# Kernel tuning notes

Hardware: AMD Instinct MI355X
Metric: run time of the kernel (lower is better)

Reference implementation:

```python
import jax, jax.numpy as jnp
import numpy as np

N, E, H = 100000, 640000, 64
DIN_N, DIN_E, L, OUT = 32, 16, 2, 1
BN_EPS = 1e-5


def setup_inputs() -> dict:
    key = jax.random.key(0)
    ks = iter(jax.random.split(key, 40))
    def p(shape, s=0.05):
        return jax.random.normal(next(ks), shape, dtype=jnp.float32) * s
    return {
        "x": jax.random.normal(next(ks), (N, DIN_N), dtype=jnp.float32),
        "edge_attr": jax.random.normal(next(ks), (E, DIN_E), dtype=jnp.float32),
        "src": jax.random.randint(next(ks), (E,), 0, N),
        "dst": jax.random.randint(next(ks), (E,), 0, N),
        "node_emb_w": p((DIN_N, H)), "node_emb_b": p((H,)),
        "edge_emb_w": p((DIN_E, H)), "edge_emb_b": p((H,)),
        "lin_edge_w": p((L, H, H)), "lin_edge_b": p((L, H)),
        "conv_w1": p((L, H, H)), "conv_b1": p((L, H)),
        "conv_w2": p((L, H, H)), "conv_b2": p((L, H)),
        "emlp_w1": p((L, 3 * H, H)), "emlp_b1": p((L, H)),
        "emlp_w2": p((L, H, H)), "emlp_b2": p((L, H)),
        "bn_gamma": jnp.ones((L, H), jnp.float32),
        "bn_beta": jnp.zeros((L, H), jnp.float32),
        "mlp_w1": p((3 * H, 50)), "mlp_b1": p((50,)),
        "mlp_w2": p((50, 25)), "mlp_b2": p((25,)),
        "mlp_w3": p((25, OUT)), "mlp_b3": p((OUT,)),
    }


def _batchnorm(h, gamma, beta):
    # training-mode BatchNorm1d over the node axis (biased variance)
    mu = jnp.mean(h, axis=0)
    var = jnp.mean(jnp.square(h - mu), axis=0)
    return gamma * (h - mu) * jax.lax.rsqrt(var + BN_EPS) + beta


def _forward(x, edge_attr, src, dst,
             node_emb_w, node_emb_b, edge_emb_w, edge_emb_b,
             lin_edge_w, lin_edge_b, conv_w1, conv_b1, conv_w2, conv_b2,
             emlp_w1, emlp_b1, emlp_w2, emlp_b2, bn_gamma, bn_beta,
             mlp_w1, mlp_b1, mlp_w2, mlp_b2, mlp_w3, mlp_b3):
    x = x @ node_emb_w + node_emb_b                       # [N, H]
    e = edge_attr @ edge_emb_w + edge_emb_b               # [E, H]
    for i in range(L):
        # GINEConv (eps=0): msg = ReLU(x_src + Lin(edge_attr)); sum at dst
        msg = jax.nn.relu(x[src] + e @ lin_edge_w[i] + lin_edge_b[i])
        agg = jax.ops.segment_sum(msg, dst, num_segments=N)
        h = x + agg
        h = jax.nn.relu(h @ conv_w1[i] + conv_b1[i]) @ conv_w2[i] + conv_b2[i]
        x = (x + jax.nn.relu(_batchnorm(h, bn_gamma[i], bn_beta[i]))) / 2
        cat = jnp.concatenate([x[src], x[dst], e], axis=-1)  # [E, 3H]
        upd = jax.nn.relu(cat @ emlp_w1[i] + emlp_b1[i]) @ emlp_w2[i] + emlp_b2[i]
        e = e + upd / 2
    # edge readout: relu(cat(x_src, x_dst)) ++ edge_attr -> MLP (dropout off/eval)
    er = jnp.concatenate(
        [jax.nn.relu(jnp.concatenate([x[src], x[dst]], axis=-1)), e], axis=-1)
    hmid = jax.nn.relu(er @ mlp_w1 + mlp_b1)
    hmid = jax.nn.relu(hmid @ mlp_w2 + mlp_b2)
    logit = hmid @ mlp_w3 + mlp_b3
    return x, logit


def reference(x, edge_attr, src, dst,
              node_emb_w, node_emb_b, edge_emb_w, edge_emb_b,
              lin_edge_w, lin_edge_b, conv_w1, conv_b1, conv_w2, conv_b2,
              emlp_w1, emlp_b1, emlp_w2, emlp_b2, bn_gamma, bn_beta,
              mlp_w1, mlp_b1, mlp_w2, mlp_b2, mlp_w3, mlp_b3):
    return _forward(x, edge_attr, src, dst,
                    node_emb_w, node_emb_b, edge_emb_w, edge_emb_b,
                    lin_edge_w, lin_edge_b, conv_w1, conv_b1, conv_w2, conv_b2,
                    emlp_w1, emlp_b1, emlp_w2, emlp_b2, bn_gamma, bn_beta,
                    mlp_w1, mlp_b1, mlp_w2, mlp_b2, mlp_w3, mlp_b3)
```

## Files before the change

### kernel.cpp

```cpp
#include <hip/hip_runtime.h>

#define NN 100000
#define NE 640000
#define NB_SCAN 98

typedef __attribute__((ext_vector_type(8))) short short8;
typedef __attribute__((ext_vector_type(4))) float f32x4;
typedef __attribute__((ext_vector_type(4))) ushort ushort4v;

__device__ __forceinline__ float bf2f(ushort u) {
    unsigned v = ((unsigned)u) << 16;
    return __builtin_bit_cast(float, v);
}
__device__ __forceinline__ ushort f2bf(float f) {
    unsigned u = __builtin_bit_cast(unsigned, f);
    u += 0x7fffu + ((u >> 16) & 1u);
    return (ushort)(u >> 16);
}
__device__ __forceinline__ short8 brelu(short8 v) {
    #pragma unroll
    for (int i = 0; i < 8; ++i) v[i] = (v[i] < (short)0) ? (short)0 : v[i];
    return v;
}

__global__ void k_hist(const int* __restrict__ dst, int* __restrict__ hist)
{
    int i = blockIdx.x * 256 + threadIdx.x;
    atomicAdd(&hist[dst[i]], 1);
}

__global__ __launch_bounds__(256) void k_scan_part(const int* __restrict__ hist,
                                                   int* __restrict__ rp,
                                                   int* __restrict__ parts)
{
    __shared__ int s[256];
    int b = blockIdx.x, t = threadIdx.x;
    int base = b * 1024 + t * 4;
    int v[4]; int sum = 0;
    #pragma unroll
    for (int i = 0; i < 4; ++i) { int idx = base + i; v[i] = (idx < NN) ? hist[idx] : 0; sum += v[i]; }
    s[t] = sum; __syncthreads();
    for (int off = 1; off < 256; off <<= 1) {
        int x = (t >= off) ? s[t - off] : 0;
        __syncthreads(); s[t] += x; __syncthreads();
    }
    int excl = s[t] - sum;
    if (t == 255) parts[b] = s[255];
    int run = excl;
    #pragma unroll
    for (int i = 0; i < 4; ++i) { int idx = base + i; if (idx < NN) rp[idx] = run; run += v[i]; }
}

__global__ void k_scan_tops(int* __restrict__ parts, int* __restrict__ rp)
{
    __shared__ int s[128];
    int t = threadIdx.x;
    int v = (t < NB_SCAN) ? parts[t] : 0;
    s[t] = v; __syncthreads();
    for (int off = 1; off < 128; off <<= 1) {
        int x = (t >= off) ? s[t - off] : 0;
        __syncthreads(); s[t] += x; __syncthreads();
    }
    parts[t] = s[t] - v;
    if (t == 0) rp[NN] = NE;
}

__global__ __launch_bounds__(256) void k_scan_add(int* __restrict__ rp,
                                                  const int* __restrict__ parts,
                                                  int* __restrict__ cursor)
{
    int i = blockIdx.x * 256 + threadIdx.x;
    if (i >= NN) return;
    int v = rp[i] + parts[i >> 10];
    rp[i] = v; cursor[i] = v;
}

__global__ void k_scatter(const int* __restrict__ dst,
                          int* __restrict__ cursor, int* __restrict__ eidx)
{
    int i = blockIdx.x * 256 + threadIdx.x;
    int d = dst[i];
    int p = atomicAdd(&cursor[d], 1);
    eidx[p] = i;
}

__global__ void k_w_subtile(const float* __restrict__ w, ushort* __restrict__ out,
                            int K, int Nin)
{
    int t = blockIdx.x * 256 + threadIdx.x;
    if (t >= K * 64) return;
    int k = t >> 6, c = t & 63;
    float v = (c < Nin) ? w[k * Nin + c] : 0.f;
    out[((k >> 3) * 64 + c) * 8 + (k & 7)] = f2bf(v);
}

__global__ void k_w_padk(const float* __restrict__ w, ushort* __restrict__ out,
                         int Kreal, int Kpad)
{
    int t = blockIdx.x * 256 + threadIdx.x;
    if (t >= Kpad * 64) return;
    int k = t >> 6, c = t & 63;
    float v = (k < Kreal) ? w[k * 64 + c] : 0.f;
    out[((k >> 3) * 64 + c) * 8 + (k & 7)] = f2bf(v);
}

__global__ void k_w_msg(const float* __restrict__ lw, ushort* __restrict__ out)
{
    int t = blockIdx.x * 256 + threadIdx.x;
    if (t >= 128 * 64) return;
    int k = t >> 6, c = t & 63;
    float v = (k < 64) ? (k == c ? 1.f : 0.f) : lw[(k - 64) * 64 + c];
    out[((k >> 3) * 64 + c) * 8 + (k & 7)] = f2bf(v);
}

__global__ __launch_bounds__(256) void k_node_emb_mfma(
    const float* __restrict__ xin, const ushort* __restrict__ ws,
    const float* __restrict__ b, float* __restrict__ xout,
    ushort* __restrict__ xb)
{
    __shared__ ushort wl[32 * 64];
    __shared__ float fbuf[4][16 * 64];
    __shared__ ushort bbuf[4][16 * 64];
    int tid = threadIdx.x;
    *(short8*)&wl[tid * 8] = *(const short8*)&ws[tid * 8];
    __syncthreads();

    int wid = tid >> 6, lane = tid & 63, c = lane & 15, kg = lane >> 4;
    int t = blockIdx.x * 4 + wid;
    if (t >= NN / 16) return;
    int n0 = t * 16;

    const float* xr = xin + (size_t)(n0 + c) * 32 + kg * 8;
    f32x4 u0 = *(const f32x4*)xr, u1 = *(const f32x4*)(xr + 4);
    short8 a;
    #pragma unroll
    for (int j = 0; j < 4; ++j) { a[j] = (short)f2bf(u0[j]); a[4 + j] = (short)f2bf(u1[j]); }

    f32x4 acc[4];
    #pragma unroll
    for (int nt = 0; nt < 4; ++nt) {
        float bv = b[nt * 16 + c];
        acc[nt] = f32x4{bv, bv, bv, bv};
        short8 bf = *(const short8*)&wl[(kg * 64 + nt * 16 + c) * 8];
        acc[nt] = __builtin_amdgcn_mfma_f32_16x16x32_bf16(a, bf, acc[nt], 0, 0, 0);
    }
    #pragma unroll
    for (int nt = 0; nt < 4; ++nt)
        #pragma unroll
        for (int i = 0; i < 4; ++i) {
            int rr = kg * 4 + i, cc = nt * 16 + c;
            float v = acc[nt][i];
            fbuf[wid][rr * 64 + cc] = v;
            bbuf[wid][rr * 64 + cc] = f2bf(v);
        }
    #pragma unroll
    for (int r = 0; r < 4; ++r) {
        int q = r * 64 + lane;
        *(f32x4*)&xout[(size_t)(n0 + (q >> 4)) * 64 + (q & 15) * 4] =
            *(f32x4*)&fbuf[wid][q * 4];
    }
    #pragma unroll
    for (int r = 0; r < 2; ++r) {
        int q = r * 64 + lane;
        *(short8*)&xb[(size_t)(n0 + (q >> 3)) * 64 + (q & 7) * 8] =
            *(short8*)&bbuf[wid][q * 8];
    }
}

__global__ __launch_bounds__(256) void k_edge_emb_fused(
    const float* __restrict__ ein, const ushort* __restrict__ ws,
    const float* __restrict__ b, ushort* __restrict__ eb,
    const ushort* __restrict__ xb, const int* __restrict__ src,
    const ushort* __restrict__ wm, const float* __restrict__ lb,
    ushort* __restrict__ msgbuf)
{
    __shared__ ushort wl[32 * 64];
    __shared__ ushort wml[128 * 64];
    __shared__ ushort bbuf[4][16 * 72];
    int tid = threadIdx.x;
    *(short8*)&wl[tid * 8] = *(const short8*)&ws[tid * 8];
    #pragma unroll
    for (int i = 0; i < 4; ++i)
        *(short8*)&wml[(i * 256 + tid) * 8] = *(const short8*)&wm[(i * 256 + tid) * 8];
    __syncthreads();

    int wid = tid >> 6, lane = tid & 63, c = lane & 15, kg = lane >> 4;
    int e0 = (blockIdx.x * 4 + wid) * 16;
    ushort* bb = bbuf[wid];

    short8 a = (short8)0;
    if (kg < 2) {
        const float* er = ein + (size_t)(e0 + c) * 16 + kg * 8;
        f32x4 u0 = *(const f32x4*)er, u1 = *(const f32x4*)(er + 4);
        #pragma unroll
        for (int j = 0; j < 4; ++j) { a[j] = (short)f2bf(u0[j]); a[4 + j] = (short)f2bf(u1[j]); }
    }
    f32x4 acc[4];
    #pragma unroll
    for (int nt = 0; nt < 4; ++nt) {
        float bv = b[nt * 16 + c];
        acc[nt] = f32x4{bv, bv, bv, bv};
        short8 bf = *(const short8*)&wl[(kg * 64 + nt * 16 + c) * 8];
        acc[nt] = __builtin_amdgcn_mfma_f32_16x16x32_bf16(a, bf, acc[nt], 0, 0, 0);
    }
    #pragma unroll
    for (int nt = 0; nt < 4; ++nt)
        #pragma unroll
        for (int i = 0; i < 4; ++i)
            bb[(kg * 4 + i) * 72 + nt * 16 + c] = f2bf(acc[nt][i]);
    #pragma unroll
    for (int r = 0; r < 2; ++r) {
        int q = r * 64 + lane;
        *(short8*)&eb[(size_t)(e0 + (q >> 3)) * 64 + (q & 7) * 8] =
            *(short8*)&bb[(q >> 3) * 72 + (q & 7) * 8];
    }
    short8 en0 = *(const short8*)&bb[c * 72 + kg * 8];
    short8 en1 = *(const short8*)&bb[c * 72 + 32 + kg * 8];
    const ushort* xs = xb + (size_t)src[e0 + c] * 64;
    short8 a0 = *(const short8*)(xs + kg * 8);
    short8 a1 = *(const short8*)(xs + 32 + kg * 8);

    f32x4 acc3[4];
    #pragma unroll
    for (int nt = 0; nt < 4; ++nt) {
        float bv = lb[nt * 16 + c];
        acc3[nt] = f32x4{bv, bv, bv, bv};
    }
    short8 af[4] = {a0, a1, en0, en1};
    #pragma unroll
    for (int ks = 0; ks < 4; ++ks) {
        #pragma unroll
        for (int nt = 0; nt < 4; ++nt) {
            short8 bf = *(const short8*)&wml[((ks * 4 + kg) * 64 + nt * 16 + c) * 8];
            acc3[nt] = __builtin_amdgcn_mfma_f32_16x16x32_bf16(af[ks], bf, acc3[nt], 0, 0, 0);
        }
    }
    #pragma unroll
    for (int nt = 0; nt < 4; ++nt)
        #pragma unroll
        for (int i = 0; i < 4; ++i)
            bb[(kg * 4 + i) * 72 + nt * 16 + c] = f2bf(fmaxf(acc3[nt][i], 0.f));
    #pragma unroll
    for (int r = 0; r < 2; ++r) {
        int q = r * 64 + lane;
        *(short8*)&msgbuf[(size_t)(e0 + (q >> 3)) * 64 + (q & 7) * 8] =
            *(short8*)&bb[(q >> 3) * 72 + (q & 7) * 8];
    }
}

__global__ __launch_bounds__(256) void k_conv_csr(
    const float* __restrict__ x, const ushort* __restrict__ msgbuf,
    const int* __restrict__ rp, const int* __restrict__ eidx,
    float* __restrict__ hout,
    const ushort* __restrict__ w1s, const float* __restrict__ b1,
    const ushort* __restrict__ w2s, const float* __restrict__ b2,
    float* __restrict__ stats)
{
    __shared__ ushort w1l[64 * 64];
    __shared__ ushort w2l[64 * 64];
    __shared__ ushort h1l[4][1024];
    __shared__ float red[2][4][64];
    int tid = threadIdx.x;
    #pragma unroll
    for (int i = 0; i < 2; ++i) {
        *(short8*)&w1l[(i * 256 + tid) * 8] = *(const short8*)&w1s[(i * 256 + tid) * 8];
        *(short8*)&w2l[(i * 256 + tid) * 8] = *(const short8*)&w2s[(i * 256 + tid) * 8];
    }
    __syncthreads();

    int wid = tid >> 6, lane = tid & 63;
    int c = lane & 15, kg = lane >> 4;

    short8 w2f[2][4];
    #pragma unroll
    for (int ks = 0; ks < 2; ++ks)
        #pragma unroll
        for (int nt = 0; nt < 4; ++nt)
            w2f[ks][nt] = *(const short8*)&w2l[((ks * 4 + kg) * 64 + nt * 16 + c) * 8];

    float b1v[4], b2v[4];
    #pragma unroll
    for (int nt = 0; nt < 4; ++nt) { b1v[nt] = b1[nt * 16 + c]; b2v[nt] = b2[nt * 16 + c]; }

    float s1[4] = {0.f, 0.f, 0.f, 0.f}, s2[4] = {0.f, 0.f, 0.f, 0.f};
    ushort* hl = h1l[wid];

    int t = blockIdx.x * 4 + wid;
    if (t < NN / 16) {
        int n0 = t * 16;
        int n = n0 + c;
        int jb = rp[n], je = rp[n + 1];
        float sm0[8] = {0,0,0,0,0,0,0,0}, sm1[8] = {0,0,0,0,0,0,0,0};
        for (int j = jb; j < je; ++j) {
            int row = eidx[j];
            short8 m0 = *(const short8*)&msgbuf[(size_t)row * 64 + kg * 8];
            short8 m1 = *(const short8*)&msgbuf[(size_t)row * 64 + 32 + kg * 8];
            #pragma unroll
            for (int i = 0; i < 8; ++i) {
                sm0[i] += bf2f((ushort)m0[i]);
                sm1[i] += bf2f((ushort)m1[i]);
            }
        }
        const float* xr = x + (size_t)n * 64;
        f32x4 u0 = *(const f32x4*)(xr + kg * 8);
        f32x4 u1 = *(const f32x4*)(xr + kg * 8 + 4);
        f32x4 v0 = *(const f32x4*)(xr + 32 + kg * 8);
        f32x4 v1 = *(const f32x4*)(xr + 32 + kg * 8 + 4);
        short8 a[2];
        #pragma unroll
        for (int j = 0; j < 4; ++j) {
            a[0][j]     = (short)f2bf(u0[j] + sm0[j]);
            a[0][4 + j] = (short)f2bf(u1[j] + sm0[4 + j]);
            a[1][j]     = (short)f2bf(v0[j] + sm1[j]);
            a[1][4 + j] = (short)f2bf(v1[j] + sm1[4 + j]);
        }
        f32x4 acc[4];
        #pragma unroll
        for (int nt = 0; nt < 4; ++nt) acc[nt] = f32x4{b1v[nt], b1v[nt], b1v[nt], b1v[nt]};
        #pragma unroll
        for (int ks = 0; ks < 2; ++ks) {
            #pragma unroll
            for (int nt = 0; nt < 4; ++nt) {
                short8 bf = *(const short8*)&w1l[((ks * 4 + kg) * 64 + nt * 16 + c) * 8];
                acc[nt] = __builtin_amdgcn_mfma_f32_16x16x32_bf16(a[ks], bf, acc[nt], 0, 0, 0);
            }
        }
        #pragma unroll
        for (int nt = 0; nt < 4; ++nt) {
            #pragma unroll
            for (int i = 0; i < 4; ++i) {
                int rr = kg * 4 + i, cc = nt * 16 + c;
                hl[((cc >> 3) * 16 + rr) * 8 + (cc & 7)] = f2bf(fmaxf(acc[nt][i], 0.f));
            }
        }
        f32x4 acc2[4];
        #pragma unroll
        for (int nt = 0; nt < 4; ++nt) acc2[nt] = f32x4{b2v[nt], b2v[nt], b2v[nt], b2v[nt]};
        #pragma unroll
        for (int ks = 0; ks < 2; ++ks) {
            short8 ha = *(const short8*)&hl[((ks * 4 + kg) * 16 + c) * 8];
            #pragma unroll
            for (int nt = 0; nt < 4; ++nt)
                acc2[nt] = __builtin_amdgcn_mfma_f32_16x16x32_bf16(ha, w2f[ks][nt], acc2[nt], 0, 0, 0);
        }
        #pragma unroll
        for (int nt = 0; nt < 4; ++nt) {
            #pragma unroll
            for (int i = 0; i < 4; ++i) {
                int rr = kg * 4 + i, cc = nt * 16 + c;
                float h2 = acc2[nt][i];
                hout[(size_t)(n0 + rr) * 64 + cc] = h2;
                s1[nt] += h2;
                s2[nt] += h2 * h2;
            }
        }
    }
    #pragma unroll
    for (int nt = 0; nt < 4; ++nt) {
        float v1 = s1[nt], v2 = s2[nt];
        v1 += __shfl_xor(v1, 16); v1 += __shfl_xor(v1, 32);
        v2 += __shfl_xor(v2, 16); v2 += __shfl_xor(v2, 32);
        s1[nt] = v1; s2[nt] = v2;
    }
    if (lane < 16) {
        #pragma unroll
        for (int nt = 0; nt < 4; ++nt) {
            red[0][wid][nt * 16 + c] = s1[nt];
            red[1][wid][nt * 16 + c] = s2[nt];
        }
    }
    __syncthreads();
    if (wid == 0) {
        float a = red[0][0][lane] + red[0][1][lane] + red[0][2][lane] + red[0][3][lane];
        float b = red[1][0][lane] + red[1][1][lane] + red[1][2][lane] + red[1][3][lane];
        unsafeAtomicAdd(&stats[lane], a);
        unsafeAtomicAdd(&stats[64 + lane], b);
    }
}

__global__ void k_bnfin(float* __restrict__ stats,
                        const float* __restrict__ gamma,
                        const float* __restrict__ beta)
{
    int j = threadIdx.x;
    float mu = stats[j] * (1.f / NN);
    float var = stats[64 + j] * (1.f / NN) - mu * mu;
    float a = gamma[j] * rsqrtf(var + 1e-5f);
    stats[128 + j] = a;
    stats[192 + j] = beta[j] - mu * a;
}

__global__ __launch_bounds__(256) void k_xupd4(float* __restrict__ x,
                                               const float* __restrict__ h,
                                               const float* __restrict__ stats,
                                               ushort* __restrict__ xb)
{
    int idx = blockIdx.x * 256 + threadIdx.x;
    int j4 = (idx & 15) * 4;
    f32x4 hv = *(const f32x4*)&h[(size_t)idx * 4];
    f32x4 xv = *(const f32x4*)&x[(size_t)idx * 4];
    f32x4 av = *(const f32x4*)&stats[128 + j4];
    f32x4 cv = *(const f32x4*)&stats[192 + j4];
    f32x4 xo;
    ushort4v bo;
    #pragma unroll
    for (int i = 0; i < 4; ++i) {
        float r = fmaxf(fmaf(hv[i], av[i], cv[i]), 0.f);
        float xn = (xv[i] + r) * 0.5f;
        xo[i] = xn;
        bo[i] = f2bf(xn);
    }
    *(f32x4*)&x[(size_t)idx * 4] = xo;
    *(ushort4v*)&xb[(size_t)idx * 4] = bo;
}

template<int NEXT>
__global__ __launch_bounds__(256) void k_emlp_fused(
    const ushort* __restrict__ xb, ushort* __restrict__ eb,
    const int* __restrict__ src, const int* __restrict__ dst,
    const ushort* __restrict__ w1s, const float* __restrict__ b1,
    const ushort* __restrict__ w2s, const float* __restrict__ b2,
    const ushort* __restrict__ wm, const float* __restrict__ lbn,
    ushort* __restrict__ msgbuf)
{
    __shared__ ushort w1l[192 * 64];
    __shared__ ushort wml[NEXT ? 128 * 64 : 8];
    __shared__ ushort hb[4][1152];
    int tid = threadIdx.x;
    #pragma unroll
    for (int i = 0; i < 6; ++i)
        *(short8*)&w1l[(i * 256 + tid) * 8] = *(const short8*)&w1s[(i * 256 + tid) * 8];
    if (NEXT) {
        #pragma unroll
        for (int i = 0; i < 4; ++i)
            *(short8*)&wml[(i * 256 + tid) * 8] = *(const short8*)&wm[(i * 256 + tid) * 8];
    }
    __syncthreads();

    int wid = tid >> 6, lane = tid & 63;
    int c = lane & 15, kg = lane >> 4;

    short8 w2f[2][4];
    #pragma unroll
    for (int ks = 0; ks < 2; ++ks)
        #pragma unroll
        for (int nt = 0; nt < 4; ++nt)
            w2f[ks][nt] = *(const short8*)&w2s[((ks * 4 + kg) * 64 + nt * 16 + c) * 8];

    float b1v[4], b2v[4], lbv[4];
    #pragma unroll
    for (int nt = 0; nt < 4; ++nt) {
        b1v[nt] = b1[nt * 16 + c];
        b2v[nt] = b2[nt * 16 + c];
        lbv[nt] = NEXT ? lbn[nt * 16 + c] : 0.f;
    }
    ushort* hl = hb[wid];

    #pragma unroll 1
    for (int t4 = 0; t4 < 4; ++t4) {
        int e0 = blockIdx.x * 256 + wid * 64 + t4 * 16;
        int myedge = e0 + c;
        int s = src[myedge], d = dst[myedge];
        const ushort* xs = xb + (size_t)s * 64;
        const ushort* xd = xb + (size_t)d * 64;
        const ushort* ee = eb + (size_t)myedge * 64;
        short8 a[6];
        a[0] = *(const short8*)(xs + kg * 8);
        a[1] = *(const short8*)(xs + 32 + kg * 8);
        a[2] = *(const short8*)(xd + kg * 8);
        a[3] = *(const short8*)(xd + 32 + kg * 8);
        a[4] = *(const short8*)(ee + kg * 8);
        a[5] = *(const short8*)(ee + 32 + kg * 8);

        f32x4 acc[4];
        #pragma unroll
        for (int nt = 0; nt < 4; ++nt) acc[nt] = f32x4{b1v[nt], b1v[nt], b1v[nt], b1v[nt]};
        #pragma unroll
        for (int ks = 0; ks < 6; ++ks) {
            #pragma unroll
            for (int nt = 0; nt < 4; ++nt) {
                short8 bf = *(const short8*)&w1l[((ks * 4 + kg) * 64 + nt * 16 + c) * 8];
                acc[nt] = __builtin_amdgcn_mfma_f32_16x16x32_bf16(a[ks], bf, acc[nt], 0, 0, 0);
            }
        }
        #pragma unroll
        for (int nt = 0; nt < 4; ++nt) {
            #pragma unroll
            for (int i = 0; i < 4; ++i) {
                int rr = kg * 4 + i, cc = nt * 16 + c;
                hl[((cc >> 3) * 16 + rr) * 8 + (cc & 7)] = f2bf(fmaxf(acc[nt][i], 0.f));
            }
        }
        f32x4 acc2[4];
        #pragma unroll
        for (int nt = 0; nt < 4; ++nt) acc2[nt] = f32x4{b2v[nt], b2v[nt], b2v[nt], b2v[nt]};
        #pragma unroll
        for (int ks = 0; ks < 2; ++ks) {
            short8 ha = *(const short8*)&hl[((ks * 4 + kg) * 16 + c) * 8];
            #pragma unroll
            for (int nt = 0; nt < 4; ++nt)
                acc2[nt] = __builtin_amdgcn_mfma_f32_16x16x32_bf16(ha, w2f[ks][nt], acc2[nt], 0, 0, 0);
        }
        #pragma unroll
        for (int nt = 0; nt < 4; ++nt)
            #pragma unroll
            for (int i = 0; i < 4; ++i)
                hl[(kg * 4 + i) * 72 + nt * 16 + c] = f2bf(acc2[nt][i]);
        short8 u0 = *(const short8*)&hl[c * 72 + kg * 8];
        short8 u1 = *(const short8*)&hl[c * 72 + 32 + kg * 8];
        short8 en0, en1;
        #pragma unroll
        for (int j = 0; j < 8; ++j) {
            en0[j] = (short)f2bf(bf2f((ushort)a[4][j]) + 0.5f * bf2f((ushort)u0[j]));
            en1[j] = (short)f2bf(bf2f((ushort)a[5][j]) + 0.5f * bf2f((ushort)u1[j]));
        }
        *(short8*)&eb[(size_t)myedge * 64 + kg * 8]      = en0;
        *(short8*)&eb[(size_t)myedge * 64 + 32 + kg * 8] = en1;

        if (NEXT) {
            f32x4 acc3[4];
            #pragma unroll
            for (int nt = 0; nt < 4; ++nt) acc3[nt] = f32x4{lbv[nt], lbv[nt], lbv[nt], lbv[nt]};
            short8 af[4] = {a[0], a[1], en0, en1};
            #pragma unroll
            for (int ks = 0; ks < 4; ++ks) {
                #pragma unroll
                for (int nt = 0; nt < 4; ++nt) {
                    short8 bf = *(const short8*)&wml[((ks * 4 + kg) * 64 + nt * 16 + c) * 8];
                    acc3[nt] = __builtin_amdgcn_mfma_f32_16x16x32_bf16(af[ks], bf, acc3[nt], 0, 0, 0);
                }
            }
            #pragma unroll
            for (int nt = 0; nt < 4; ++nt)
                #pragma unroll
                for (int i = 0; i < 4; ++i)
                    hl[(kg * 4 + i) * 72 + nt * 16 + c] = f2bf(fmaxf(acc3[nt][i], 0.f));
            #pragma unroll
            for (int r = 0; r < 2; ++r) {
                int q = r * 64 + lane;
                *(short8*)&msgbuf[(size_t)(e0 + (q >> 3)) * 64 + (q & 7) * 8] =
                    *(short8*)&hl[(q >> 3) * 72 + (q & 7) * 8];
            }
        }
    }
}

__global__ __launch_bounds__(256) void k_readout_mfma(
    const ushort* __restrict__ xb, const ushort* __restrict__ eb,
    const int* __restrict__ src, const int* __restrict__ dst,
    const ushort* __restrict__ w1s, const float* __restrict__ b1,
    const float* __restrict__ w2, const float* __restrict__ b2,
    const float* __restrict__ w3, const float* __restrict__ b3,
    float* __restrict__ logit)
{
    __shared__ ushort w1l[192 * 64];
    __shared__ ushort hw[4][64 * 50];
    int tid = threadIdx.x;
    #pragma unroll
    for (int i = 0; i < 6; ++i)
        *(short8*)&w1l[(i * 256 + tid) * 8] = *(const short8*)&w1s[(i * 256 + tid) * 8];
    __syncthreads();

    int wid = tid >> 6, lane = tid & 63;
    int c = lane & 15, kg = lane >> 4;
    float b1v[4];
    #pragma unroll
    for (int nt = 0; nt < 4; ++nt) b1v[nt] = (nt * 16 + c < 50) ? b1[nt * 16 + c] : 0.f;

    #pragma unroll 1
    for (int t4 = 0; t4 < 4; ++t4) {
        int e0 = blockIdx.x * 256 + wid * 64 + t4 * 16;
        int myedge = e0 + c;
        int s = src[myedge], d = dst[myedge];
        const ushort* xs = xb + (size_t)s * 64;
        const ushort* xd = xb + (size_t)d * 64;
        const ushort* ee = eb + (size_t)myedge * 64;
        short8 a[6];
        a[0] = brelu(*(const short8*)(xs + kg * 8));
        a[1] = brelu(*(const short8*)(xs + 32 + kg * 8));
        a[2] = brelu(*(const short8*)(xd + kg * 8));
        a[3] = brelu(*(const short8*)(xd + 32 + kg * 8));
        a[4] = *(const short8*)(ee + kg * 8);
        a[5] = *(const short8*)(ee + 32 + kg * 8);

        f32x4 acc[4];
        #pragma unroll
        for (int nt = 0; nt < 4; ++nt) acc[nt] = f32x4{b1v[nt], b1v[nt], b1v[nt], b1v[nt]};
        #pragma unroll
        for (int ks = 0; ks < 6; ++ks) {
            #pragma unroll
            for (int nt = 0; nt < 4; ++nt) {
                short8 bf = *(const short8*)&w1l[((ks * 4 + kg) * 64 + nt * 16 + c) * 8];
                acc[nt] = __builtin_amdgcn_mfma_f32_16x16x32_bf16(a[ks], bf, acc[nt], 0, 0, 0);
            }
        }
        #pragma unroll
        for (int nt = 0; nt < 4; ++nt) {
            #pragma unroll
            for (int i = 0; i < 4; ++i) {
                int rr = kg * 4 + i, cc = nt * 16 + c;
                if (cc < 50)
                    hw[wid][(t4 * 16 + rr) * 50 + cc] = f2bf(fmaxf(acc[nt][i], 0.f));
            }
        }
    }
    int edge = blockIdx.x * 256 + wid * 64 + lane;
    const ushort* hrow = &hw[wid][lane * 50];
    float a25[25];
    #pragma unroll
    for (int j = 0; j < 25; ++j) a25[j] = b2[j];
    #pragma unroll 2
    for (int k = 0; k < 50; ++k) {
        float hv = bf2f(hrow[k]);
        #pragma unroll
        for (int j = 0; j < 25; ++j) a25[j] = fmaf(hv, w2[k * 25 + j], a25[j]);
    }
    float lg = b3[0];
    #pragma unroll
    for (int k = 0; k < 25; ++k) lg = fmaf(fmaxf(a25[k], 0.f), w3[k], lg);
    logit[edge] = lg;
}

extern "C" void kernel_launch(void* const* d_in, const int* in_sizes, int n_in,
                              void* d_out, int out_size, void* d_ws, size_t ws_size,
                              hipStream_t stream)
{
    const float* x_in  = (const float*)d_in[0];
    const float* eattr = (const float*)d_in[1];
    const int*   src   = (const int*)d_in[2];
    const int*   dst   = (const int*)d_in[3];
    const float* n_w   = (const float*)d_in[4];
    const float* n_b   = (const float*)d_in[5];
    const float* e_w   = (const float*)d_in[6];
    const float* e_b   = (const float*)d_in[7];
    const float* lw    = (const float*)d_in[8];
    const float* lb    = (const float*)d_in[9];
    const float* cw1   = (const float*)d_in[10];
    const float* cb1   = (const float*)d_in[11];
    const float* cw2   = (const float*)d_in[12];
    const float* cb2   = (const float*)d_in[13];
    const float* ew1   = (const float*)d_in[14];
    const float* eb1   = (const float*)d_in[15];
    const float* ew2   = (const float*)d_in[16];
    const float* eb2   = (const float*)d_in[17];
    const float* gam   = (const float*)d_in[18];
    const float* bet   = (const float*)d_in[19];
    const float* m1w   = (const float*)d_in[20];
    const float* m1b   = (const float*)d_in[21];
    const float* m2w   = (const float*)d_in[22];
    const float* m2b   = (const float*)d_in[23];
    const float* m3w   = (const float*)d_in[24];
    const float* m3b   = (const float*)d_in[25];

    float* xbuf  = (float*)d_out;
    float* logit = xbuf + (size_t)NN * 64;

    ushort* eb     = (ushort*)d_ws;
    float*  tmp    = (float*)(eb + (size_t)NE * 64);
    float*  stats  = tmp + (size_t)NN * 64;
    ushort* w1s    = (ushort*)(stats + 256);
    ushort* w2s    = w1s + 2 * 192 * 64;
    ushort* m1s    = w2s + 2 * 64 * 64;
    ushort* xb     = m1s + 192 * 64;
    ushort* wms    = xb + (size_t)NN * 64;
    ushort* cw1s   = wms + 2 * 128 * 64;
    ushort* cw2s   = cw1s + 2 * 64 * 64;
    ushort* nws    = cw2s + 2 * 64 * 64;
    ushort* ews    = nws + 32 * 64;
    ushort* msgbuf = ews + 32 * 64;
    int*    hist   = (int*)(msgbuf + (size_t)NE * 64);
    int*    rp     = hist + NN;
    int*    cursor = rp + NN + 1;
    int*    parts  = cursor + NN;
    int*    eidx   = parts + 128;

    hipMemsetAsync(hist, 0, NN * sizeof(int), stream);
    k_hist<<<NE / 256, 256, 0, stream>>>(dst, hist);
    k_scan_part<<<NB_SCAN, 256, 0, stream>>>(hist, rp, parts);
    k_scan_tops<<<1, 128, 0, stream>>>(parts, rp);
    k_scan_add<<<(NN + 255) / 256, 256, 0, stream>>>(rp, parts, cursor);
    k_scatter<<<NE / 256, 256, 0, stream>>>(dst, cursor, eidx);

    k_w_subtile<<<48, 256, 0, stream>>>(ew1,            w1s,            192, 64);
    k_w_subtile<<<48, 256, 0, stream>>>(ew1 + 192 * 64, w1s + 192 * 64, 192, 64);
    k_w_subtile<<<16, 256, 0, stream>>>(ew2,            w2s,            64, 64);
    k_w_subtile<<<16, 256, 0, stream>>>(ew2 + 64 * 64,  w2s + 64 * 64,  64, 64);
    k_w_subtile<<<48, 256, 0, stream>>>(m1w,            m1s,            192, 50);
    k_w_msg<<<32, 256, 0, stream>>>(lw,           wms);
    k_w_msg<<<32, 256, 0, stream>>>(lw + 64 * 64, wms + 128 * 64);
    k_w_subtile<<<16, 256, 0, stream>>>(cw1,            cw1s,           64, 64);
    k_w_subtile<<<16, 256, 0, stream>>>(cw1 + 64 * 64,  cw1s + 64 * 64, 64, 64);
    k_w_subtile<<<16, 256, 0, stream>>>(cw2,            cw2s,           64, 64);
    k_w_subtile<<<16, 256, 0, stream>>>(cw2 + 64 * 64,  cw2s + 64 * 64, 64, 64);
    k_w_padk<<<8, 256, 0, stream>>>(n_w, nws, 32, 32);
    k_w_padk<<<8, 256, 0, stream>>>(e_w, ews, 16, 32);

    k_node_emb_mfma<<<(NN / 16 + 3) / 4, 256, 0, stream>>>(x_in, nws, n_b, xbuf, xb);
    k_edge_emb_fused<<<NE / 64, 256, 0, stream>>>(eattr, ews, e_b, eb,
                                                  xb, src, wms, lb, msgbuf);

    for (int l = 0; l < 2; ++l) {
        hipMemsetAsync(stats, 0, 256 * sizeof(float), stream);
        k_conv_csr<<<(NN / 16 + 3) / 4, 256, 0, stream>>>(
            xbuf, msgbuf, rp, eidx, tmp, cw1s + l * 64 * 64, cb1 + l * 64,
            cw2s + l * 64 * 64, cb2 + l * 64, stats);
        k_bnfin<<<1, 64, 0, stream>>>(stats, gam + l * 64, bet + l * 64);
        k_xupd4<<<NN * 16 / 256, 256, 0, stream>>>(xbuf, tmp, stats, xb);
        if (l == 0) {
            k_emlp_fused<1><<<NE / 256, 256, 0, stream>>>(
                xb, eb, src, dst, w1s, eb1, w2s, eb2,
                wms + 128 * 64, lb + 64, msgbuf);
        } else {
            k_emlp_fused<0><<<NE / 256, 256, 0, stream>>>(
                xb, eb, src, dst, w1s + 192 * 64, eb1 + 64, w2s + 64 * 64, eb2 + 64,
                wms, lb, msgbuf);
        }
    }

    k_readout_mfma<<<NE / 256, 256, 0, stream>>>(xb, eb, src, dst,
                                                 m1s, m1b, m2w, m2b, m3w, m3b, logit);
}
```

Baseline: 571.9 us.

## Store edge data in dst-sorted order and enlarge emlp blocks to 512 threads

Edge arrays (edge embeddings, messages, src/dst indices) are now kept in CSR (dst-sorted) order. Sorted copies of src and dst are built during the scatter, and logits are written back through eidx. The aggregation then reads messages contiguously with no indirection, and the x[dst] gathers hit mostly the same rows. The edge-MLP kernel also moves to 512-thread blocks so each block loads its weights into LDS once for twice as many edges. The cost is extra scatter writes and a scattered logit store.

```diff
diff --git a/kernel.cpp b/kernel.cpp
--- a/kernel.cpp
+++ b/kernel.cpp
@@ -75,13 +75,14 @@
     rp[i] = v; cursor[i] = v;
 }
 
-__global__ void k_scatter(const int* __restrict__ dst,
-                          int* __restrict__ cursor, int* __restrict__ eidx)
+__global__ void k_scatter(const int* __restrict__ src, const int* __restrict__ dst,
+                          int* __restrict__ cursor, int* __restrict__ eidx,
+                          int* __restrict__ ssrc, int* __restrict__ sdst)
 {
     int i = blockIdx.x * 256 + threadIdx.x;
     int d = dst[i];
     int p = atomicAdd(&cursor[d], 1);
-    eidx[p] = i;
+    eidx[p] = i; ssrc[p] = src[i]; sdst[p] = d;
 }
 
 __global__ void k_w_subtile(const float* __restrict__ w, ushort* __restrict__ out,
@@ -170,9 +171,9 @@
 __global__ __launch_bounds__(256) void k_edge_emb_fused(
     const float* __restrict__ ein, const ushort* __restrict__ ws,
     const float* __restrict__ b, ushort* __restrict__ eb,
-    const ushort* __restrict__ xb, const int* __restrict__ src,
-    const ushort* __restrict__ wm, const float* __restrict__ lb,
-    ushort* __restrict__ msgbuf)
+    const ushort* __restrict__ xb, const int* __restrict__ ssrc,
+    const int* __restrict__ eidx, const ushort* __restrict__ wm,
+    const float* __restrict__ lb, ushort* __restrict__ msgbuf)
 {
     __shared__ ushort wl[32 * 64];
     __shared__ ushort wml[128 * 64];
@@ -185,12 +186,13 @@
     __syncthreads();
 
     int wid = tid >> 6, lane = tid & 63, c = lane & 15, kg = lane >> 4;
-    int e0 = (blockIdx.x * 4 + wid) * 16;
+    int p0 = (blockIdx.x * 4 + wid) * 16;
     ushort* bb = bbuf[wid];
 
     short8 a = (short8)0;
     if (kg < 2) {
-        const float* er = ein + (size_t)(e0 + c) * 16 + kg * 8;
+        int orig = eidx[p0 + c];
+        const float* er = ein + (size_t)orig * 16 + kg * 8;
         f32x4 u0 = *(const f32x4*)er, u1 = *(const f32x4*)(er + 4);
         #pragma unroll
         for (int j = 0; j < 4; ++j) { a[j] = (short)f2bf(u0[j]); a[4 + j] = (short)f2bf(u1[j]); }
@@ -211,12 +213,12 @@
     #pragma unroll
     for (int r = 0; r < 2; ++r) {
         int q = r * 64 + lane;
-        *(short8*)&eb[(size_t)(e0 + (q >> 3)) * 64 + (q & 7) * 8] =
+        *(short8*)&eb[(size_t)(p0 + (q >> 3)) * 64 + (q & 7) * 8] =
             *(short8*)&bb[(q >> 3) * 72 + (q & 7) * 8];
     }
     short8 en0 = *(const short8*)&bb[c * 72 + kg * 8];
     short8 en1 = *(const short8*)&bb[c * 72 + 32 + kg * 8];
-    const ushort* xs = xb + (size_t)src[e0 + c] * 64;
+    const ushort* xs = xb + (size_t)ssrc[p0 + c] * 64;
     short8 a0 = *(const short8*)(xs + kg * 8);
     short8 a1 = *(const short8*)(xs + 32 + kg * 8);
 
@@ -243,15 +245,14 @@
     #pragma unroll
     for (int r = 0; r < 2; ++r) {
         int q = r * 64 + lane;
-        *(short8*)&msgbuf[(size_t)(e0 + (q >> 3)) * 64 + (q & 7) * 8] =
+        *(short8*)&msgbuf[(size_t)(p0 + (q >> 3)) * 64 + (q & 7) * 8] =
             *(short8*)&bb[(q >> 3) * 72 + (q & 7) * 8];
     }
 }
 
 __global__ __launch_bounds__(256) void k_conv_csr(
     const float* __restrict__ x, const ushort* __restrict__ msgbuf,
-    const int* __restrict__ rp, const int* __restrict__ eidx,
-    float* __restrict__ hout,
+    const int* __restrict__ rp, float* __restrict__ hout,
     const ushort* __restrict__ w1s, const float* __restrict__ b1,
     const ushort* __restrict__ w2s, const float* __restrict__ b2,
     float* __restrict__ stats)
@@ -292,9 +293,8 @@
         int jb = rp[n], je = rp[n + 1];
         float sm0[8] = {0,0,0,0,0,0,0,0}, sm1[8] = {0,0,0,0,0,0,0,0};
         for (int j = jb; j < je; ++j) {
-            int row = eidx[j];
-            short8 m0 = *(const short8*)&msgbuf[(size_t)row * 64 + kg * 8];
-            short8 m1 = *(const short8*)&msgbuf[(size_t)row * 64 + 32 + kg * 8];
+            short8 m0 = *(const short8*)&msgbuf[(size_t)j * 64 + kg * 8];
+            short8 m1 = *(const short8*)&msgbuf[(size_t)j * 64 + 32 + kg * 8];
             #pragma unroll
             for (int i = 0; i < 8; ++i) {
                 sm0[i] += bf2f((ushort)m0[i]);
@@ -415,9 +415,9 @@
 }
 
 template<int NEXT>
-__global__ __launch_bounds__(256) void k_emlp_fused(
+__global__ __launch_bounds__(512) void k_emlp_fused(
     const ushort* __restrict__ xb, ushort* __restrict__ eb,
-    const int* __restrict__ src, const int* __restrict__ dst,
+    const int* __restrict__ ssrc, const int* __restrict__ sdst,
     const ushort* __restrict__ w1s, const float* __restrict__ b1,
     const ushort* __restrict__ w2s, const float* __restrict__ b2,
     const ushort* __restrict__ wm, const float* __restrict__ lbn,
@@ -425,15 +425,15 @@
 {
     __shared__ ushort w1l[192 * 64];
     __shared__ ushort wml[NEXT ? 128 * 64 : 8];
-    __shared__ ushort hb[4][1152];
+    __shared__ ushort hb[8][1152];
     int tid = threadIdx.x;
     #pragma unroll
-    for (int i = 0; i < 6; ++i)
-        *(short8*)&w1l[(i * 256 + tid) * 8] = *(const short8*)&w1s[(i * 256 + tid) * 8];
+    for (int i = 0; i < 3; ++i)
+        *(short8*)&w1l[(i * 512 + tid) * 8] = *(const short8*)&w1s[(i * 512 + tid) * 8];
     if (NEXT) {
         #pragma unroll
-        for (int i = 0; i < 4; ++i)
-            *(short8*)&wml[(i * 256 + tid) * 8] = *(const short8*)&wm[(i * 256 + tid) * 8];
+        for (int i = 0; i < 2; ++i)
+            *(short8*)&wml[(i * 512 + tid) * 8] = *(const short8*)&wm[(i * 512 + tid) * 8];
     }
     __syncthreads();
 
@@ -458,12 +458,12 @@
 
     #pragma unroll 1
     for (int t4 = 0; t4 < 4; ++t4) {
-        int e0 = blockIdx.x * 256 + wid * 64 + t4 * 16;
-        int myedge = e0 + c;
-        int s = src[myedge], d = dst[myedge];
+        int p0 = blockIdx.x * 512 + wid * 64 + t4 * 16;
+        int myp = p0 + c;
+        int s = ssrc[myp], d = sdst[myp];
         const ushort* xs = xb + (size_t)s * 64;
         const ushort* xd = xb + (size_t)d * 64;
-        const ushort* ee = eb + (size_t)myedge * 64;
+        const ushort* ee = eb + (size_t)myp * 64;
         short8 a[6];
         a[0] = *(const short8*)(xs + kg * 8);
         a[1] = *(const short8*)(xs + 32 + kg * 8);
@@ -514,8 +514,8 @@
             en0[j] = (short)f2bf(bf2f((ushort)a[4][j]) + 0.5f * bf2f((ushort)u0[j]));
             en1[j] = (short)f2bf(bf2f((ushort)a[5][j]) + 0.5f * bf2f((ushort)u1[j]));
         }
-        *(short8*)&eb[(size_t)myedge * 64 + kg * 8]      = en0;
-        *(short8*)&eb[(size_t)myedge * 64 + 32 + kg * 8] = en1;
+        *(short8*)&eb[(size_t)myp * 64 + kg * 8]      = en0;
+        *(short8*)&eb[(size_t)myp * 64 + 32 + kg * 8] = en1;
 
         if (NEXT) {
             f32x4 acc3[4];
@@ -538,7 +538,7 @@
             #pragma unroll
             for (int r = 0; r < 2; ++r) {
                 int q = r * 64 + lane;
-                *(short8*)&msgbuf[(size_t)(e0 + (q >> 3)) * 64 + (q & 7) * 8] =
+                *(short8*)&msgbuf[(size_t)(p0 + (q >> 3)) * 64 + (q & 7) * 8] =
                     *(short8*)&hl[(q >> 3) * 72 + (q & 7) * 8];
             }
         }
@@ -547,7 +547,8 @@
 
 __global__ __launch_bounds__(256) void k_readout_mfma(
     const ushort* __restrict__ xb, const ushort* __restrict__ eb,
-    const int* __restrict__ src, const int* __restrict__ dst,
+    const int* __restrict__ ssrc, const int* __restrict__ sdst,
+    const int* __restrict__ eidx,
     const ushort* __restrict__ w1s, const float* __restrict__ b1,
     const float* __restrict__ w2, const float* __restrict__ b2,
     const float* __restrict__ w3, const float* __restrict__ b3,
@@ -569,12 +570,12 @@
 
     #pragma unroll 1
     for (int t4 = 0; t4 < 4; ++t4) {
-        int e0 = blockIdx.x * 256 + wid * 64 + t4 * 16;
-        int myedge = e0 + c;
-        int s = src[myedge], d = dst[myedge];
+        int p0 = blockIdx.x * 256 + wid * 64 + t4 * 16;
+        int myp = p0 + c;
+        int s = ssrc[myp], d = sdst[myp];
         const ushort* xs = xb + (size_t)s * 64;
         const ushort* xd = xb + (size_t)d * 64;
-        const ushort* ee = eb + (size_t)myedge * 64;
+        const ushort* ee = eb + (size_t)myp * 64;
         short8 a[6];
         a[0] = brelu(*(const short8*)(xs + kg * 8));
         a[1] = brelu(*(const short8*)(xs + 32 + kg * 8));
@@ -604,7 +605,7 @@
             }
         }
     }
-    int edge = blockIdx.x * 256 + wid * 64 + lane;
+    int p = blockIdx.x * 256 + wid * 64 + lane;
     const ushort* hrow = &hw[wid][lane * 50];
     float a25[25];
     #pragma unroll
@@ -618,7 +619,7 @@
     float lg = b3[0];
     #pragma unroll
     for (int k = 0; k < 25; ++k) lg = fmaf(fmaxf(a25[k], 0.f), w3[k], lg);
-    logit[edge] = lg;
+    logit[eidx[p]] = lg;
 }
 
 extern "C" void kernel_launch(void* const* d_in, const int* in_sizes, int n_in,
@@ -673,13 +674,15 @@
     int*    cursor = rp + NN + 1;
     int*    parts  = cursor + NN;
     int*    eidx   = parts + 128;
+    int*    ssrc   = eidx + NE;
+    int*    sdst   = ssrc + NE;
 
     hipMemsetAsync(hist, 0, NN * sizeof(int), stream);
     k_hist<<<NE / 256, 256, 0, stream>>>(dst, hist);
     k_scan_part<<<NB_SCAN, 256, 0, stream>>>(hist, rp, parts);
     k_scan_tops<<<1, 128, 0, stream>>>(parts, rp);
     k_scan_add<<<(NN + 255) / 256, 256, 0, stream>>>(rp, parts, cursor);
-    k_scatter<<<NE / 256, 256, 0, stream>>>(dst, cursor, eidx);
+    k_scatter<<<NE / 256, 256, 0, stream>>>(src, dst, cursor, eidx, ssrc, sdst);
 
     k_w_subtile<<<48, 256, 0, stream>>>(ew1,            w1s,            192, 64);
     k_w_subtile<<<48, 256, 0, stream>>>(ew1 + 192 * 64, w1s + 192 * 64, 192, 64);
@@ -697,26 +700,26 @@
 
     k_node_emb_mfma<<<(NN / 16 + 3) / 4, 256, 0, stream>>>(x_in, nws, n_b, xbuf, xb);
     k_edge_emb_fused<<<NE / 64, 256, 0, stream>>>(eattr, ews, e_b, eb,
-                                                  xb, src, wms, lb, msgbuf);
+                                                  xb, ssrc, eidx, wms, lb, msgbuf);
 
     for (int l = 0; l < 2; ++l) {
         hipMemsetAsync(stats, 0, 256 * sizeof(float), stream);
         k_conv_csr<<<(NN / 16 + 3) / 4, 256, 0, stream>>>(
-            xbuf, msgbuf, rp, eidx, tmp, cw1s + l * 64 * 64, cb1 + l * 64,
+            xbuf, msgbuf, rp, tmp, cw1s + l * 64 * 64, cb1 + l * 64,
             cw2s + l * 64 * 64, cb2 + l * 64, stats);
         k_bnfin<<<1, 64, 0, stream>>>(stats, gam + l * 64, bet + l * 64);
         k_xupd4<<<NN * 16 / 256, 256, 0, stream>>>(xbuf, tmp, stats, xb);
         if (l == 0) {
-            k_emlp_fused<1><<<NE / 256, 256, 0, stream>>>(
-                xb, eb, src, dst, w1s, eb1, w2s, eb2,
+            k_emlp_fused<1><<<NE / 512, 512, 0, stream>>>(
+                xb, eb, ssrc, sdst, w1s, eb1, w2s, eb2,
                 wms + 128 * 64, lb + 64, msgbuf);
         } else {
-            k_emlp_fused<0><<<NE / 256, 256, 0, stream>>>(
-                xb, eb, src, dst, w1s + 192 * 64, eb1 + 64, w2s + 64 * 64, eb2 + 64,
+            k_emlp_fused<0><<<NE / 512, 512, 0, stream>>>(
+                xb, eb, ssrc, sdst, w1s + 192 * 64, eb1 + 64, w2s + 64 * 64, eb2 + 64,
                 wms, lb, msgbuf);
         }
     }
 
-    k_readout_mfma<<<NE / 256, 256, 0, stream>>>(xb, eb, src, dst,
+    k_readout_mfma<<<NE / 256, 256, 0, stream>>>(xb, eb, ssrc, sdst, eidx,
                                                  m1s, m1b, m2w, m2b, m3w, m3b, logit);
 }
```

Measured after the change: 626.9 us. +9.6%, slower.
